# Kernel tuning notes

Measured on AMD Instinct MI355X. Metric: run time of the kernel, lower is better.

The kernel has to match this reference:

```python
import jax, jax.numpy as jnp
import numpy as np

B, NV, FD = 16, 128, 8192
T_TEMP = 0.2      # self.T
MARGIN = 1.0      # nn.TripletMarginLoss default
EPS = 1e-6        # pairwise_distance eps


def _l2norm(x):
    # torch F.normalize(dim=1): x / max(||x||, 1e-12)
    nrm = jnp.maximum(jnp.linalg.norm(x, axis=-1, keepdims=True), 1e-12)
    return x / nrm


def _ssl_parts(qb, kb, nb, num_gt):
    # qb,kb,nb: [NV, FD] flattened reid embeddings for one image
    qv = _l2norm(qb)[:num_gt]          # [g, FD]
    kv = _l2norm(kb)[:num_gt]          # [g, FD]
    nv = _l2norm(nb)                   # [NV, FD] (negatives are NOT sliced)
    g = num_gt
    S = qv @ kv.T                      # [g, g] all pairwise dots (replaces torch.dot loops)
    # similarity-matrix loss
    sm = jnp.sum((S - jnp.eye(g, dtype=S.dtype)) ** 2) / (g * g)
    # pairwise distances with torch eps convention: ||a - b + eps||_2
    # = sqrt(||a||^2 + ||b||^2 - 2 a.b + 2*eps*(sum(a)-sum(b)) + D*eps^2); ||a||=||b||=1
    sq = qv.sum(axis=1)                # [g]
    sk = kv.sum(axis=1)                # [g]
    const = FD * EPS * EPS
    d_qk = jnp.sqrt(jnp.maximum(2.0 - 2.0 * S + 2.0 * EPS * (sq[:, None] - sk[None, :]) + const, 0.0))
    d_kq = jnp.sqrt(jnp.maximum(2.0 - 2.0 * S.T + 2.0 * EPS * (sk[:, None] - sq[None, :]) + const, 0.0))
    off = 1.0 - jnp.eye(g, dtype=S.dtype)
    # triplet: anc=q_i,pos=k_i,neg=k_j  and  anc=k_i,pos=q_i,neg=q_j, j != i
    tri1 = jnp.sum(jax.nn.relu(jnp.diag(d_qk)[:, None] - d_qk + MARGIN) * off)
    tri2 = jnp.sum(jax.nn.relu(jnp.diag(d_kq)[:, None] - d_kq + MARGIN) * off)
    tri_sum = tri1 + tri2
    # cycle consistency: |q_i.k_j - k_i.q_j| = |S[i,j] - S[j,i]|
    cyc = jnp.sum(jnp.abs(S - S.T) * off) / (g * (g - 1))
    # InfoNCE: l_pos = q_i.k_i, l_neg = q @ n.T
    l_pos = jnp.diag(S)[:, None]       # [g, 1]
    l_neg = qv @ nv.T                  # [g, NV]
    logits = jnp.concatenate([l_pos, l_neg], axis=1) / T_TEMP
    ce = jnp.mean(jax.nn.logsumexp(logits, axis=1) - logits[:, 0])  # CE with labels=0
    return sm, tri_sum, cyc, ce / g


def setup_inputs() -> dict:
    key = jax.random.key(0)
    kq, kk, kn = jax.random.split(key, 3)
    q = jax.random.normal(kq, (B, NV, FD), dtype=jnp.float32)
    k = jax.random.normal(kk, (B, NV, FD), dtype=jnp.float32)
    n = jax.random.normal(kn, (B, NV, FD), dtype=jnp.float32)
    return {"q": q, "k": k, "n": n, "num_gt": NV}


def reference(q, k, n, num_gt):
    sm, tri, cyc, ce = jax.vmap(lambda a, b, c: _ssl_parts(a, b, c, num_gt))(q, k, n)
    tri_cnt = 2 * num_gt * (num_gt - 1)
    # original bug: tri_loss accumulates across batches while tri_cnt resets,
    # so each batch contributes cumsum(tri)[b] / tri_cnt
    ssl = jnp.sum(sm) + jnp.sum(jnp.cumsum(tri)) / tri_cnt + jnp.sum(cyc) + jnp.sum(ce)
    return ssl
```

## Files before the change

kernel.cpp:

```cpp
#include <hip/hip_runtime.h>
#include <cstdint>
#include <cstddef>

#define B_N   16
#define G_N   128
#define FD_N  8192
#define KSPLIT 16
#define KC    512
#define BK2   32
#define NITER 16

typedef unsigned short u16;
typedef u16  u16x4 __attribute__((ext_vector_type(4)));
typedef u16  u16x8 __attribute__((ext_vector_type(8)));
typedef __bf16 bf16x8 __attribute__((ext_vector_type(8)));
typedef float f32x16 __attribute__((ext_vector_type(16)));

#define QSUM_P   0
#define QSSQ_P   32768
#define KSUM_P   65536
#define KSSQ_P   98304
#define NSSQ_P   131072
#define SM_ROW   163840
#define CE_ROW   165888
#define S_OFF    167936
#define PART_OFF_F 430080

__device__ __forceinline__ u16 f2bf(float f) {
    uint32_t u = __float_as_uint(f);
    u += 0x7FFFu + ((u >> 16) & 1u);
    return (u16)(u >> 16);
}

#define LDS_BARRIER() asm volatile("s_waitcnt lgkmcnt(0)\n\ts_barrier" ::: "memory")

__global__ __launch_bounds__(512, 4)
void k_gemm(const float* __restrict__ q, const float* __restrict__ kM,
            const float* __restrict__ nM, float* __restrict__ ws)
{
    __shared__ __align__(16) u16 sA[G_N * BK2];
    __shared__ __align__(16) u16 sB[G_N * BK2];

    const int tid = threadIdx.x;
    const int blk = blockIdx.x;
    const int b    = blk >> 5;
    const int rem  = blk & 31;
    const int half = rem >> 4;
    const int kch  = rem & 15;

    const int r0 = tid >> 3;
    const int c8 = tid & 7;

    const size_t mat_off = (size_t)b * (G_N * FD_N) + (size_t)kch * KC + (size_t)(c8 * 4);
    const float* Ap = q + mat_off;
    const float* Bp = (half ? nM : kM) + mat_off;

    float4 a0[2], b0[2], a1[2], b1[2];
    float aS[2] = {0,0}, aQ[2] = {0,0}, bS[2] = {0,0}, bQ[2] = {0,0};

    #pragma unroll
    for (int i = 0; i < 2; ++i) {
        size_t ro = (size_t)(r0 + 64*i) * FD_N;
        a0[i] = *(const float4*)(Ap + ro);
        b0[i] = *(const float4*)(Bp + ro);
    }
    #pragma unroll
    for (int i = 0; i < 2; ++i) {
        size_t ro = (size_t)(r0 + 64*i) * FD_N + BK2;
        a1[i] = *(const float4*)(Ap + ro);
        b1[i] = *(const float4*)(Bp + ro);
    }

    const int lane  = tid & 63;
    const int wv    = tid >> 6;
    const int wm    = wv >> 2;
    const int wn    = wv & 3;
    const int khalf = lane >> 5;
    const int lrow  = lane & 31;
    const int rA0 = wm*64 + lrow;
    const int rB0 = wn*32 + lrow;

    int wof[2];
    #pragma unroll
    for (int i = 0; i < 2; ++i) {
        int row = r0 + 64*i;
        wof[i] = row*BK2 + 8*((c8>>1) ^ ((row>>1)&3)) + 4*(c8&1);
    }

    f32x16 acc[2];
    #pragma unroll
    for (int mb = 0; mb < 2; ++mb)
      #pragma unroll
      for (int e = 0; e < 16; ++e) acc[mb][e] = 0.f;

#define STORE_STAGE(AR, BR)                                                   \
    {                                                                         \
        _Pragma("unroll")                                                     \
        for (int i = 0; i < 2; ++i) {                                         \
            float4 v = AR[i];                                                 \
            aS[i] += v.x + v.y + v.z + v.w;                                   \
            aQ[i] += v.x*v.x + v.y*v.y + v.z*v.z + v.w*v.w;                   \
            u16x4 h; h[0]=f2bf(v.x); h[1]=f2bf(v.y); h[2]=f2bf(v.z); h[3]=f2bf(v.w); \
            *(u16x4*)(sA + wof[i]) = h;                                       \
            v = BR[i];                                                        \
            bS[i] += v.x + v.y + v.z + v.w;                                   \
            bQ[i] += v.x*v.x + v.y*v.y + v.z*v.z + v.w*v.w;                   \
            u16x4 h2; h2[0]=f2bf(v.x); h2[1]=f2bf(v.y); h2[2]=f2bf(v.z); h2[3]=f2bf(v.w); \
            *(u16x4*)(sB + wof[i]) = h2;                                      \
        }                                                                     \
    }

#define REFILL(AR, BR, KOFF)                                                  \
    {                                                                         \
        _Pragma("unroll")                                                     \
        for (int i = 0; i < 2; ++i) {                                         \
            size_t ro = (size_t)(r0 + 64*i) * FD_N + (KOFF);                  \
            AR[i] = *(const float4*)(Ap + ro);                                \
            BR[i] = *(const float4*)(Bp + ro);                                \
        }                                                                     \
    }

#define MFMA_PHASE()                                                          \
    {                                                                         \
        _Pragma("unroll")                                                     \
        for (int s = 0; s < 2; ++s) {                                         \
            int chunk = s*2 + khalf;                                          \
            bf16x8 af0, af1, bfv;                                             \
            { int row = rA0;                                                  \
              u16x8 raw = *(const u16x8*)(sA + row*BK2 + 8*(chunk ^ ((row>>1)&3))); \
              af0 = __builtin_bit_cast(bf16x8, raw); }                        \
            { int row = rA0 + 32;                                             \
              u16x8 raw = *(const u16x8*)(sA + row*BK2 + 8*(chunk ^ ((row>>1)&3))); \
              af1 = __builtin_bit_cast(bf16x8, raw); }                        \
            { int row = rB0;                                                  \
              u16x8 raw = *(const u16x8*)(sB + row*BK2 + 8*(chunk ^ ((row>>1)&3))); \
              bfv = __builtin_bit_cast(bf16x8, raw); }                        \
            acc[0] = __builtin_amdgcn_mfma_f32_32x32x16_bf16(af0, bfv, acc[0], 0, 0, 0); \
            acc[1] = __builtin_amdgcn_mfma_f32_32x32x16_bf16(af1, bfv, acc[1], 0, 0, 0); \
        }                                                                     \
    }

    for (int kb = 0; kb < NITER; kb += 2) {
        LDS_BARRIER();
        STORE_STAGE(a0, b0);
        LDS_BARRIER();
        if (kb + 2 < NITER) REFILL(a0, b0, (size_t)(kb+2)*BK2);
        MFMA_PHASE();
        LDS_BARRIER();
        STORE_STAGE(a1, b1);
        LDS_BARRIER();
        if (kb + 3 < NITER) REFILL(a1, b1, (size_t)(kb+3)*BK2);
        MFMA_PHASE();
    }

    u16* part = (u16*)(ws + PART_OFF_F) + ((size_t)blk << 14);
    #pragma unroll
    for (int mb = 0; mb < 2; ++mb) {
        int col = wn*32 + lrow;
        int rbase = wm*64 + mb*32 + 4*khalf;
        #pragma unroll
        for (int reg = 0; reg < 16; ++reg) {
            int row = rbase + (reg & 3) + 8*(reg >> 2);
            part[row*G_N + col] = f2bf(acc[mb][reg]);
        }
    }

    #pragma unroll
    for (int i = 0; i < 2; ++i) {
        float sa = aS[i], qa = aQ[i], sb = bS[i], qb = bQ[i];
        #pragma unroll
        for (int m = 4; m >= 1; m >>= 1) {
            sa += __shfl_xor(sa, m, 64); qa += __shfl_xor(qa, m, 64);
            sb += __shfl_xor(sb, m, 64); qb += __shfl_xor(qb, m, 64);
        }
        if (c8 == 0) {
            int o = kch*2048 + b*G_N + (r0 + 64*i);
            if (half == 0) {
                ws[QSUM_P + o] = sa; ws[QSSQ_P + o] = qa;
                ws[KSUM_P + o] = sb; ws[KSSQ_P + o] = qb;
            } else {
                ws[NSSQ_P + o] = qb;
            }
        }
    }
}

__global__ __launch_bounds__(256)
void k_red2(float* __restrict__ ws, float* __restrict__ out)
{
    const int blk  = blockIdx.x;
    const int b    = blk >> 4;
    const int half = (blk >> 3) & 1;
    const int rg   = blk & 7;
    const int t    = threadIdx.x;
    const int lr   = t >> 4;
    const int i    = rg*16 + lr;
    const int c8   = t & 15;
    __shared__ float nrm[128];
    __shared__ float invq_s[16];

    if (blk == 0 && t == 0) out[0] = 0.f;

    if (t < 128) {
        float ss = 0.f;
        const float* p = ws + (half ? NSSQ_P : KSSQ_P) + b*G_N + t;
        #pragma unroll
        for (int kc2 = 0; kc2 < KSPLIT; ++kc2) ss += p[kc2*2048];
        nrm[t] = 1.f / fmaxf(sqrtf(ss), 1e-12f);
    } else if (t < 144) {
        float ss = 0.f;
        const float* p = ws + QSSQ_P + b*G_N + rg*16 + (t - 128);
        #pragma unroll
        for (int kc2 = 0; kc2 < KSPLIT; ++kc2) ss += p[kc2*2048];
        invq_s[t-128] = 1.f / fmaxf(sqrtf(ss), 1e-12f);
    }
    __syncthreads();

    const u16* part = (const u16*)(ws + PART_OFF_F);
    float s[8] = {0,0,0,0,0,0,0,0};
    #pragma unroll
    for (int kc2 = 0; kc2 < KSPLIT; ++kc2) {
        size_t idx = ((size_t)(b*32 + half*16 + kc2) << 14) + i*G_N + c8*8;
        u16x8 h = *(const u16x8*)(part + idx);
        #pragma unroll
        for (int e = 0; e < 8; ++e)
            s[e] += __uint_as_float(((uint32_t)h[e]) << 16);
    }
    const float iq = invq_s[lr];
    if (half == 0) {
        float smacc = 0.f;
        float S8[8];
        #pragma unroll
        for (int e = 0; e < 8; ++e) {
            int j = c8*8 + e;
            S8[e] = s[e] * iq * nrm[j];
            float d = S8[e] - (j == i ? 1.f : 0.f);
            smacc += d*d;
        }
        float* Sp = ws + S_OFF + (size_t)b*16384 + i*G_N + c8*8;
        float4 w0 = {S8[0],S8[1],S8[2],S8[3]};
        float4 w1 = {S8[4],S8[5],S8[6],S8[7]};
        *(float4*)Sp = w0; *(float4*)(Sp+4) = w1;
        #pragma unroll
        for (int m = 8; m >= 1; m >>= 1) smacc += __shfl_xor(smacc, m, 64);
        if (c8 == 0) ws[SM_ROW + b*G_N + i] = smacc;
    } else {
        float eacc = 0.f;
        #pragma unroll
        for (int e = 0; e < 8; ++e)
            eacc += __expf(5.f * s[e] * iq * nrm[c8*8+e]);
        #pragma unroll
        for (int m = 8; m >= 1; m >>= 1) eacc += __shfl_xor(eacc, m, 64);
        if (c8 == 0) ws[CE_ROW + b*G_N + i] = eacc;
    }
}

__global__ __launch_bounds__(256)
void k_epi(float* __restrict__ ws, float* __restrict__ out)
{
    const int blk = blockIdx.x;
    const int b   = blk >> 3;
    const int i0  = (blk & 7) * 16;
    const int t   = threadIdx.x;
    __shared__ float sqv[128], skv[128], ddq[128], ddk[128];
    __shared__ float rbuf[4];
    const float c0 = (float)FD_N * 1e-6f * 1e-6f;

    const float* S = ws + S_OFF + (size_t)b * 16384;
    if (t < 128) {
        float qs=0, qq=0, ks=0, kq=0;
        #pragma unroll
        for (int kc2 = 0; kc2 < KSPLIT; ++kc2) {
            int o = kc2*2048 + b*G_N + t;
            qs += ws[QSUM_P + o]; qq += ws[QSSQ_P + o];
            ks += ws[KSUM_P + o]; kq += ws[KSSQ_P + o];
        }
        float iq = 1.f/fmaxf(sqrtf(qq),1e-12f);
        float ik = 1.f/fmaxf(sqrtf(kq),1e-12f);
        float sq = qs*iq, sk = ks*ik;
        sqv[t]=sq; skv[t]=sk;
        float Stt = S[t*G_N + t];
        ddq[t] = sqrtf(fmaxf(2.f - 2.f*Stt + 2e-6f*(sq-sk) + c0, 0.f));
        ddk[t] = sqrtf(fmaxf(2.f - 2.f*Stt + 2e-6f*(sk-sq) + c0, 0.f));
    }
    __syncthreads();

    float tri=0.f, cyc=0.f, ce=0.f, sm=0.f;
    #pragma unroll
    for (int p = 0; p < 8; ++p) {
        int idx = p*256 + t;
        int i = i0 + (idx >> 7), j = idx & 127;
        if (i != j) {
            float S_ij = S[i*G_N + j];
            float dqk = sqrtf(fmaxf(2.f - 2.f*S_ij + 2e-6f*(sqv[i]-skv[j]) + c0, 0.f));
            tri += fmaxf(ddq[i] - dqk + 1.f, 0.f);
            float dkq = sqrtf(fmaxf(2.f - 2.f*S_ij + 2e-6f*(skv[j]-sqv[i]) + c0, 0.f));
            tri += fmaxf(ddk[j] - dkq + 1.f, 0.f);
            cyc += fabsf(S_ij - S[j*G_N + i]);
        }
    }
    if (t < 16) {
        int r = i0 + t;
        float lp = 5.f * S[r*G_N + r];
        ce = __logf(ws[CE_ROW + b*G_N + r] + __expf(lp)) - lp;
        sm = ws[SM_ROW + b*G_N + r];
    }
    float contrib = sm * (1.f/16384.f) + cyc * (1.f/16256.f) + ce * (1.f/16384.f)
                  + (float)(B_N - b) * tri * (1.f/32512.f);
    #pragma unroll
    for (int m = 32; m >= 1; m >>= 1) contrib += __shfl_xor(contrib, m, 64);
    if ((t & 63) == 0) rbuf[t >> 6] = contrib;
    __syncthreads();
    if (t == 0) atomicAdd(out, rbuf[0] + rbuf[1] + rbuf[2] + rbuf[3]);
}

extern "C" void kernel_launch(void* const* d_in, const int* in_sizes, int n_in,
                              void* d_out, int out_size, void* d_ws, size_t ws_size,
                              hipStream_t stream)
{
    const float* q  = (const float*)d_in[0];
    const float* kM = (const float*)d_in[1];
    const float* nM = (const float*)d_in[2];
    float* ws  = (float*)d_ws;
    float* out = (float*)d_out;

    k_gemm<<<B_N * 2 * KSPLIT, 512, 0, stream>>>(q, kM, nM, ws);
    k_red2<<<256, 256, 0, stream>>>(ws, out);
    k_epi<<<128, 256, 0, stream>>>(ws, out);
}
```

Before: 219.2 us.

## Stream fp32 tiles to LDS via global_load_lds with double buffering

Result: no change. 219.6 us (+0.2%).

```diff
diff --git a/kernel.cpp b/kernel.cpp
--- a/kernel.cpp
+++ b/kernel.cpp
@@ -11,7 +11,6 @@
 #define NITER 16
 
 typedef unsigned short u16;
-typedef u16  u16x4 __attribute__((ext_vector_type(4)));
 typedef u16  u16x8 __attribute__((ext_vector_type(8)));
 typedef __bf16 bf16x8 __attribute__((ext_vector_type(8)));
 typedef float f32x16 __attribute__((ext_vector_type(16)));
@@ -32,14 +31,22 @@
     return (u16)(u >> 16);
 }
 
-#define LDS_BARRIER() asm volatile("s_waitcnt lgkmcnt(0)\n\ts_barrier" ::: "memory")
+__device__ __forceinline__ void load_lds16(const float* g, float* l) {
+    __builtin_amdgcn_global_load_lds(
+        (__attribute__((address_space(1))) void*)(g),
+        (__attribute__((address_space(3))) void*)(l),
+        16, 0, 0);
+}
+
+#define WAITV4() asm volatile("s_waitcnt vmcnt(4)" ::: "memory")
+#define WAITV0() asm volatile("s_waitcnt vmcnt(0)" ::: "memory")
 
 __global__ __launch_bounds__(512, 4)
 void k_gemm(const float* __restrict__ q, const float* __restrict__ kM,
             const float* __restrict__ nM, float* __restrict__ ws)
 {
-    __shared__ __align__(16) u16 sA[G_N * BK2];
-    __shared__ __align__(16) u16 sB[G_N * BK2];
+    __shared__ __align__(16) float sA[2][G_N * BK2];
+    __shared__ __align__(16) float sB[2][G_N * BK2];
 
     const int tid = threadIdx.x;
     const int blk = blockIdx.x;
@@ -47,29 +54,6 @@
     const int rem  = blk & 31;
     const int half = rem >> 4;
     const int kch  = rem & 15;
-
-    const int r0 = tid >> 3;
-    const int c8 = tid & 7;
-
-    const size_t mat_off = (size_t)b * (G_N * FD_N) + (size_t)kch * KC + (size_t)(c8 * 4);
-    const float* Ap = q + mat_off;
-    const float* Bp = (half ? nM : kM) + mat_off;
-
-    float4 a0[2], b0[2], a1[2], b1[2];
-    float aS[2] = {0,0}, aQ[2] = {0,0}, bS[2] = {0,0}, bQ[2] = {0,0};
-
-    #pragma unroll
-    for (int i = 0; i < 2; ++i) {
-        size_t ro = (size_t)(r0 + 64*i) * FD_N;
-        a0[i] = *(const float4*)(Ap + ro);
-        b0[i] = *(const float4*)(Bp + ro);
-    }
-    #pragma unroll
-    for (int i = 0; i < 2; ++i) {
-        size_t ro = (size_t)(r0 + 64*i) * FD_N + BK2;
-        a1[i] = *(const float4*)(Ap + ro);
-        b1[i] = *(const float4*)(Bp + ro);
-    }
 
     const int lane  = tid & 63;
     const int wv    = tid >> 6;
@@ -79,13 +63,61 @@
     const int lrow  = lane & 31;
     const int rA0 = wm*64 + lrow;
     const int rB0 = wn*32 + lrow;
-
-    int wof[2];
-    #pragma unroll
-    for (int i = 0; i < 2; ++i) {
-        int row = r0 + 64*i;
-        wof[i] = row*BK2 + 8*((c8>>1) ^ ((row>>1)&3)) + 4*(c8&1);
-    }
+    const bool statA = (wn == 0);
+    const bool statB = (wm == 0);
+
+    const size_t mat_off = (size_t)b * (G_N * FD_N) + (size_t)kch * KC;
+    const float* Ap = q + mat_off;
+    const float* Bp = (half ? nM : kM) + mat_off;
+
+    const int r0s = wv*16 + (lane >> 3);
+    const int r1s = r0s + 8;
+    const size_t goff0 = (size_t)r0s * FD_N + (size_t)(((lane & 7) ^ (r0s & 7)) << 2);
+    const size_t goff1 = (size_t)r1s * FD_N + (size_t)(((lane & 7) ^ (r1s & 7)) << 2);
+    const int lds0 = wv * 512;
+    const int lds1 = wv * 512 + 256;
+
+#define STAGE(ST, T) do {                                                     \
+        const size_t tof_ = (size_t)((T) * BK2);                              \
+        load_lds16(Ap + goff0 + tof_, &sA[ST][lds0]);                         \
+        load_lds16(Bp + goff0 + tof_, &sB[ST][lds0]);                         \
+        load_lds16(Ap + goff1 + tof_, &sA[ST][lds1]);                         \
+        load_lds16(Bp + goff1 + tof_, &sB[ST][lds1]);                         \
+    } while (0)
+
+#define LOADCVT(SP, R, CH, FR, EN, SS, QQ) do {                               \
+        const int x_ = (R) & 7;                                               \
+        const float* rp_ = (SP) + (R) * BK2;                                  \
+        float4 lo_ = *(const float4*)(rp_ + ((((CH)*2    ) ^ x_) << 2));      \
+        float4 hi_ = *(const float4*)(rp_ + ((((CH)*2 + 1) ^ x_) << 2));      \
+        if (EN) {                                                             \
+            SS += (lo_.x + lo_.y) + (lo_.z + lo_.w)                           \
+                + (hi_.x + hi_.y) + (hi_.z + hi_.w);                          \
+            QQ += lo_.x*lo_.x + lo_.y*lo_.y + lo_.z*lo_.z + lo_.w*lo_.w       \
+                + hi_.x*hi_.x + hi_.y*hi_.y + hi_.z*hi_.z + hi_.w*hi_.w;      \
+        }                                                                     \
+        u16x8 h_;                                                             \
+        h_[0]=f2bf(lo_.x); h_[1]=f2bf(lo_.y); h_[2]=f2bf(lo_.z); h_[3]=f2bf(lo_.w); \
+        h_[4]=f2bf(hi_.x); h_[5]=f2bf(hi_.y); h_[6]=f2bf(hi_.z); h_[7]=f2bf(hi_.w); \
+        FR = __builtin_bit_cast(bf16x8, h_);                                  \
+    } while (0)
+
+#define COMPUTE_PHASE(ST) do {                                                \
+        const float* sAp_ = &sA[ST][0];                                       \
+        const float* sBp_ = &sB[ST][0];                                       \
+        _Pragma("unroll")                                                     \
+        for (int s = 0; s < 2; ++s) {                                         \
+            const int ch = s*2 + khalf;                                       \
+            bf16x8 af0, af1, bfv;                                             \
+            LOADCVT(sAp_, rA0,      ch, af0, statA, aS0, aQ0);                \
+            LOADCVT(sAp_, rA0 + 32, ch, af1, statA, aS1, aQ1);                \
+            LOADCVT(sBp_, rB0,      ch, bfv, statB, bS0, bQ0);                \
+            acc[0] = __builtin_amdgcn_mfma_f32_32x32x16_bf16(af0, bfv, acc[0], 0, 0, 0); \
+            acc[1] = __builtin_amdgcn_mfma_f32_32x32x16_bf16(af1, bfv, acc[1], 0, 0, 0); \
+        }                                                                     \
+    } while (0)
+
+    float aS0 = 0.f, aQ0 = 0.f, aS1 = 0.f, aQ1 = 0.f, bS0 = 0.f, bQ0 = 0.f;
 
     f32x16 acc[2];
     #pragma unroll
@@ -93,65 +125,29 @@
       #pragma unroll
       for (int e = 0; e < 16; ++e) acc[mb][e] = 0.f;
 
-#define STORE_STAGE(AR, BR)                                                   \
-    {                                                                         \
-        _Pragma("unroll")                                                     \
-        for (int i = 0; i < 2; ++i) {                                         \
-            float4 v = AR[i];                                                 \
-            aS[i] += v.x + v.y + v.z + v.w;                                   \
-            aQ[i] += v.x*v.x + v.y*v.y + v.z*v.z + v.w*v.w;                   \
-            u16x4 h; h[0]=f2bf(v.x); h[1]=f2bf(v.y); h[2]=f2bf(v.z); h[3]=f2bf(v.w); \
-            *(u16x4*)(sA + wof[i]) = h;                                       \
-            v = BR[i];                                                        \
-            bS[i] += v.x + v.y + v.z + v.w;                                   \
-            bQ[i] += v.x*v.x + v.y*v.y + v.z*v.z + v.w*v.w;                   \
-            u16x4 h2; h2[0]=f2bf(v.x); h2[1]=f2bf(v.y); h2[2]=f2bf(v.z); h2[3]=f2bf(v.w); \
-            *(u16x4*)(sB + wof[i]) = h2;                                      \
-        }                                                                     \
-    }
-
-#define REFILL(AR, BR, KOFF)                                                  \
-    {                                                                         \
-        _Pragma("unroll")                                                     \
-        for (int i = 0; i < 2; ++i) {                                         \
-            size_t ro = (size_t)(r0 + 64*i) * FD_N + (KOFF);                  \
-            AR[i] = *(const float4*)(Ap + ro);                                \
-            BR[i] = *(const float4*)(Bp + ro);                                \
-        }                                                                     \
-    }
-
-#define MFMA_PHASE()                                                          \
-    {                                                                         \
-        _Pragma("unroll")                                                     \
-        for (int s = 0; s < 2; ++s) {                                         \
-            int chunk = s*2 + khalf;                                          \
-            bf16x8 af0, af1, bfv;                                             \
-            { int row = rA0;                                                  \
-              u16x8 raw = *(const u16x8*)(sA + row*BK2 + 8*(chunk ^ ((row>>1)&3))); \
-              af0 = __builtin_bit_cast(bf16x8, raw); }                        \
-            { int row = rA0 + 32;                                             \
-              u16x8 raw = *(const u16x8*)(sA + row*BK2 + 8*(chunk ^ ((row>>1)&3))); \
-              af1 = __builtin_bit_cast(bf16x8, raw); }                        \
-            { int row = rB0;                                                  \
-              u16x8 raw = *(const u16x8*)(sB + row*BK2 + 8*(chunk ^ ((row>>1)&3))); \
-              bfv = __builtin_bit_cast(bf16x8, raw); }                        \
-            acc[0] = __builtin_amdgcn_mfma_f32_32x32x16_bf16(af0, bfv, acc[0], 0, 0, 0); \
-            acc[1] = __builtin_amdgcn_mfma_f32_32x32x16_bf16(af1, bfv, acc[1], 0, 0, 0); \
-        }                                                                     \
-    }
-
-    for (int kb = 0; kb < NITER; kb += 2) {
-        LDS_BARRIER();
-        STORE_STAGE(a0, b0);
-        LDS_BARRIER();
-        if (kb + 2 < NITER) REFILL(a0, b0, (size_t)(kb+2)*BK2);
-        MFMA_PHASE();
-        LDS_BARRIER();
-        STORE_STAGE(a1, b1);
-        LDS_BARRIER();
-        if (kb + 3 < NITER) REFILL(a1, b1, (size_t)(kb+3)*BK2);
-        MFMA_PHASE();
-    }
+    STAGE(0, 0);
+    STAGE(1, 1);
+
+    for (int t = 0; t < 14; t += 2) {
+        WAITV4();
+        __builtin_amdgcn_s_barrier();
+        COMPUTE_PHASE(0);
+        __builtin_amdgcn_s_barrier();
+        STAGE(0, t + 2);
+
+        WAITV4();
+        __builtin_amdgcn_s_barrier();
+        COMPUTE_PHASE(1);
+        __builtin_amdgcn_s_barrier();
+        STAGE(1, t + 3);
+    }
+    WAITV4();
+    __builtin_amdgcn_s_barrier();
+    COMPUTE_PHASE(0);
+    __builtin_amdgcn_s_barrier();
+    WAITV0();
+    __builtin_amdgcn_s_barrier();
+    COMPUTE_PHASE(1);
 
     u16* part = (u16*)(ws + PART_OFF_F) + ((size_t)blk << 14);
     #pragma unroll
@@ -165,24 +161,26 @@
         }
     }
 
-    #pragma unroll
-    for (int i = 0; i < 2; ++i) {
-        float sa = aS[i], qa = aQ[i], sb = bS[i], qb = bQ[i];
-        #pragma unroll
-        for (int m = 4; m >= 1; m >>= 1) {
-            sa += __shfl_xor(sa, m, 64); qa += __shfl_xor(qa, m, 64);
-            sb += __shfl_xor(sb, m, 64); qb += __shfl_xor(qb, m, 64);
-        }
-        if (c8 == 0) {
-            int o = kch*2048 + b*G_N + (r0 + 64*i);
-            if (half == 0) {
-                ws[QSUM_P + o] = sa; ws[QSSQ_P + o] = qa;
-                ws[KSUM_P + o] = sb; ws[KSSQ_P + o] = qb;
-            } else {
-                ws[NSSQ_P + o] = qb;
-            }
-        }
-    }
+    if (statA) {
+        aS0 += __shfl_xor(aS0, 32, 64); aQ0 += __shfl_xor(aQ0, 32, 64);
+        aS1 += __shfl_xor(aS1, 32, 64); aQ1 += __shfl_xor(aQ1, 32, 64);
+        if (half == 0 && khalf == 0) {
+            int o = kch*2048 + b*G_N + wm*64 + lrow;
+            ws[QSUM_P + o]      = aS0; ws[QSSQ_P + o]      = aQ0;
+            ws[QSUM_P + o + 32] = aS1; ws[QSSQ_P + o + 32] = aQ1;
+        }
+    }
+    if (statB) {
+        bS0 += __shfl_xor(bS0, 32, 64); bQ0 += __shfl_xor(bQ0, 32, 64);
+        if (khalf == 0) {
+            int o = kch*2048 + b*G_N + wn*32 + lrow;
+            if (half == 0) { ws[KSUM_P + o] = bS0; ws[KSSQ_P + o] = bQ0; }
+            else           { ws[NSSQ_P + o] = bQ0; }
+        }
+    }
+#undef STAGE
+#undef LOADCVT
+#undef COMPUTE_PHASE
 }
 
 __global__ __launch_bounds__(256)
```

## Fuse q·kᵀ and q·nᵀ into one block tile to read q once

Applied to the files above, without the earlier changes.

Result: no change. 220.0 us (+0.4%).

```diff
diff --git a/kernel.cpp b/kernel.cpp
--- a/kernel.cpp
+++ b/kernel.cpp
@@ -7,11 +7,10 @@
 #define FD_N  8192
 #define KSPLIT 16
 #define KC    512
-#define BK2   32
-#define NITER 16
+#define BK    64
+#define NSTAGE 8
 
 typedef unsigned short u16;
-typedef u16  u16x4 __attribute__((ext_vector_type(4)));
 typedef u16  u16x8 __attribute__((ext_vector_type(8)));
 typedef __bf16 bf16x8 __attribute__((ext_vector_type(8)));
 typedef float f32x16 __attribute__((ext_vector_type(16)));
@@ -32,44 +31,19 @@
     return (u16)(u >> 16);
 }
 
-#define LDS_BARRIER() asm volatile("s_waitcnt lgkmcnt(0)\n\ts_barrier" ::: "memory")
-
-__global__ __launch_bounds__(512, 4)
+#define LGKM0_BAR() do { asm volatile("s_waitcnt lgkmcnt(0)" ::: "memory"); \
+                         __builtin_amdgcn_s_barrier(); } while (0)
+
+__global__ __launch_bounds__(512, 2)
 void k_gemm(const float* __restrict__ q, const float* __restrict__ kM,
             const float* __restrict__ nM, float* __restrict__ ws)
 {
-    __shared__ __align__(16) u16 sA[G_N * BK2];
-    __shared__ __align__(16) u16 sB[G_N * BK2];
+    __shared__ __align__(16) u16 smem[2 * 24576];
 
     const int tid = threadIdx.x;
     const int blk = blockIdx.x;
-    const int b    = blk >> 5;
-    const int rem  = blk & 31;
-    const int half = rem >> 4;
-    const int kch  = rem & 15;
-
-    const int r0 = tid >> 3;
-    const int c8 = tid & 7;
-
-    const size_t mat_off = (size_t)b * (G_N * FD_N) + (size_t)kch * KC + (size_t)(c8 * 4);
-    const float* Ap = q + mat_off;
-    const float* Bp = (half ? nM : kM) + mat_off;
-
-    float4 a0[2], b0[2], a1[2], b1[2];
-    float aS[2] = {0,0}, aQ[2] = {0,0}, bS[2] = {0,0}, bQ[2] = {0,0};
-
-    #pragma unroll
-    for (int i = 0; i < 2; ++i) {
-        size_t ro = (size_t)(r0 + 64*i) * FD_N;
-        a0[i] = *(const float4*)(Ap + ro);
-        b0[i] = *(const float4*)(Bp + ro);
-    }
-    #pragma unroll
-    for (int i = 0; i < 2; ++i) {
-        size_t ro = (size_t)(r0 + 64*i) * FD_N + BK2;
-        a1[i] = *(const float4*)(Ap + ro);
-        b1[i] = *(const float4*)(Bp + ro);
-    }
+    const int b   = blk >> 4;
+    const int kch = blk & 15;
 
     const int lane  = tid & 63;
     const int wv    = tid >> 6;
@@ -77,112 +51,147 @@
     const int wn    = wv & 3;
     const int khalf = lane >> 5;
     const int lrow  = lane & 31;
-    const int rA0 = wm*64 + lrow;
-    const int rB0 = wn*32 + lrow;
-
-    int wof[2];
-    #pragma unroll
-    for (int i = 0; i < 2; ++i) {
-        int row = r0 + 64*i;
-        wof[i] = row*BK2 + 8*((c8>>1) ^ ((row>>1)&3)) + 4*(c8&1);
-    }
-
-    f32x16 acc[2];
-    #pragma unroll
-    for (int mb = 0; mb < 2; ++mb)
+    const int g     = lane >> 4;
+    const int cc    = lane & 15;
+
+    const size_t mat_off = (size_t)b * (G_N * FD_N) + (size_t)kch * KC;
+    const float* Ap = q + mat_off;
+    const float* Bw = (wv < 4 ? kM : nM) + mat_off;
+
+    float4 La[4], Lb[8];
+    float sA_[4] = {0,0,0,0}, qA_[4] = {0,0,0,0};
+    float sB_[8] = {0,0,0,0,0,0,0,0}, qB_[8] = {0,0,0,0,0,0,0,0};
+
+    f32x16 acc[2][2];
+    #pragma unroll
+    for (int m = 0; m < 2; ++m)
       #pragma unroll
-      for (int e = 0; e < 16; ++e) acc[mb][e] = 0.f;
-
-#define STORE_STAGE(AR, BR)                                                   \
-    {                                                                         \
-        _Pragma("unroll")                                                     \
-        for (int i = 0; i < 2; ++i) {                                         \
-            float4 v = AR[i];                                                 \
-            aS[i] += v.x + v.y + v.z + v.w;                                   \
-            aQ[i] += v.x*v.x + v.y*v.y + v.z*v.z + v.w*v.w;                   \
-            u16x4 h; h[0]=f2bf(v.x); h[1]=f2bf(v.y); h[2]=f2bf(v.z); h[3]=f2bf(v.w); \
-            *(u16x4*)(sA + wof[i]) = h;                                       \
-            v = BR[i];                                                        \
-            bS[i] += v.x + v.y + v.z + v.w;                                   \
-            bQ[i] += v.x*v.x + v.y*v.y + v.z*v.z + v.w*v.w;                   \
-            u16x4 h2; h2[0]=f2bf(v.x); h2[1]=f2bf(v.y); h2[2]=f2bf(v.z); h2[3]=f2bf(v.w); \
-            *(u16x4*)(sB + wof[i]) = h2;                                      \
-        }                                                                     \
-    }
-
-#define REFILL(AR, BR, KOFF)                                                  \
-    {                                                                         \
-        _Pragma("unroll")                                                     \
-        for (int i = 0; i < 2; ++i) {                                         \
-            size_t ro = (size_t)(r0 + 64*i) * FD_N + (KOFF);                  \
-            AR[i] = *(const float4*)(Ap + ro);                                \
-            BR[i] = *(const float4*)(Bp + ro);                                \
-        }                                                                     \
-    }
-
-#define MFMA_PHASE()                                                          \
-    {                                                                         \
-        _Pragma("unroll")                                                     \
-        for (int s = 0; s < 2; ++s) {                                         \
-            int chunk = s*2 + khalf;                                          \
-            bf16x8 af0, af1, bfv;                                             \
-            { int row = rA0;                                                  \
-              u16x8 raw = *(const u16x8*)(sA + row*BK2 + 8*(chunk ^ ((row>>1)&3))); \
-              af0 = __builtin_bit_cast(bf16x8, raw); }                        \
-            { int row = rA0 + 32;                                             \
-              u16x8 raw = *(const u16x8*)(sA + row*BK2 + 8*(chunk ^ ((row>>1)&3))); \
-              af1 = __builtin_bit_cast(bf16x8, raw); }                        \
-            { int row = rB0;                                                  \
-              u16x8 raw = *(const u16x8*)(sB + row*BK2 + 8*(chunk ^ ((row>>1)&3))); \
-              bfv = __builtin_bit_cast(bf16x8, raw); }                        \
-            acc[0] = __builtin_amdgcn_mfma_f32_32x32x16_bf16(af0, bfv, acc[0], 0, 0, 0); \
-            acc[1] = __builtin_amdgcn_mfma_f32_32x32x16_bf16(af1, bfv, acc[1], 0, 0, 0); \
-        }                                                                     \
-    }
-
-    for (int kb = 0; kb < NITER; kb += 2) {
-        LDS_BARRIER();
-        STORE_STAGE(a0, b0);
-        LDS_BARRIER();
-        if (kb + 2 < NITER) REFILL(a0, b0, (size_t)(kb+2)*BK2);
-        MFMA_PHASE();
-        LDS_BARRIER();
-        STORE_STAGE(a1, b1);
-        LDS_BARRIER();
-        if (kb + 3 < NITER) REFILL(a1, b1, (size_t)(kb+3)*BK2);
-        MFMA_PHASE();
-    }
-
-    u16* part = (u16*)(ws + PART_OFF_F) + ((size_t)blk << 14);
-    #pragma unroll
-    for (int mb = 0; mb < 2; ++mb) {
-        int col = wn*32 + lrow;
-        int rbase = wm*64 + mb*32 + 4*khalf;
+      for (int n = 0; n < 2; ++n)
+        #pragma unroll
+        for (int e = 0; e < 16; ++e) acc[m][n][e] = 0.f;
+
+#define ISSUE(S) do {                                                          \
+        const size_t ko_ = (size_t)((S)*BK + cc*4);                            \
+        _Pragma("unroll")                                                      \
+        for (int i = 0; i < 4; ++i)                                            \
+            La[i] = *(const float4*)(Ap + (size_t)(wv*16 + i*4 + g)*FD_N + ko_); \
+        _Pragma("unroll")                                                      \
+        for (int i = 0; i < 8; ++i)                                            \
+            Lb[i] = *(const float4*)(Bw + (size_t)(wn*32 + i*4 + g)*FD_N + ko_); \
+    } while (0)
+
+#define CVTWRITE(BUF) do {                                                     \
+        u16* dA_ = smem + (BUF)*24576;                                         \
+        u16* dB_ = dA_ + 8192;                                                 \
+        _Pragma("unroll")                                                      \
+        for (int i = 0; i < 4; ++i) {                                          \
+            const int r_ = wv*16 + i*4 + g;                                    \
+            float4 v = La[i];                                                  \
+            sA_[i] += (v.x + v.y) + (v.z + v.w);                               \
+            qA_[i] += v.x*v.x + v.y*v.y + v.z*v.z + v.w*v.w;                   \
+            uint2 p;                                                           \
+            p.x = (uint32_t)f2bf(v.x) | ((uint32_t)f2bf(v.y) << 16);           \
+            p.y = (uint32_t)f2bf(v.z) | ((uint32_t)f2bf(v.w) << 16);           \
+            *(uint2*)(dA_ + r_*64 + ((cc ^ ((r_&7)<<1)) << 2)) = p;            \
+        }                                                                      \
+        _Pragma("unroll")                                                      \
+        for (int i = 0; i < 8; ++i) {                                          \
+            const int r_  = wn*32 + i*4 + g;                                   \
+            const int rl_ = r_ + (wv < 4 ? 0 : 128);                           \
+            float4 v = Lb[i];                                                  \
+            sB_[i] += (v.x + v.y) + (v.z + v.w);                               \
+            qB_[i] += v.x*v.x + v.y*v.y + v.z*v.z + v.w*v.w;                   \
+            uint2 p;                                                           \
+            p.x = (uint32_t)f2bf(v.x) | ((uint32_t)f2bf(v.y) << 16);           \
+            p.y = (uint32_t)f2bf(v.z) | ((uint32_t)f2bf(v.w) << 16);           \
+            *(uint2*)(dB_ + rl_*64 + ((cc ^ ((rl_&7)<<1)) << 2)) = p;          \
+        }                                                                      \
+    } while (0)
+
+#define FRAG(DP, R, KCH)                                                       \
+    __builtin_bit_cast(bf16x8, *(const u16x8*)((DP) + (R)*64 +                 \
+        ((((KCH)*2 + khalf) ^ ((R)&7)) << 3)))
+
+#define COMPUTE(BUF) do {                                                      \
+        const u16* dA_ = smem + (BUF)*24576;                                   \
+        const u16* dB_ = dA_ + 8192;                                           \
+        __builtin_amdgcn_s_setprio(1);                                         \
+        _Pragma("unroll")                                                      \
+        for (int kc = 0; kc < 4; ++kc) {                                       \
+            bf16x8 a0_ = FRAG(dA_, wm*64 +      lrow, kc);                     \
+            bf16x8 a1_ = FRAG(dA_, wm*64 + 32 + lrow, kc);                     \
+            bf16x8 b0_ = FRAG(dB_, wn*64 +      lrow, kc);                     \
+            bf16x8 b1_ = FRAG(dB_, wn*64 + 32 + lrow, kc);                     \
+            acc[0][0] = __builtin_amdgcn_mfma_f32_32x32x16_bf16(a0_, b0_, acc[0][0], 0,0,0); \
+            acc[0][1] = __builtin_amdgcn_mfma_f32_32x32x16_bf16(a0_, b1_, acc[0][1], 0,0,0); \
+            acc[1][0] = __builtin_amdgcn_mfma_f32_32x32x16_bf16(a1_, b0_, acc[1][0], 0,0,0); \
+            acc[1][1] = __builtin_amdgcn_mfma_f32_32x32x16_bf16(a1_, b1_, acc[1][1], 0,0,0); \
+        }                                                                      \
+        __builtin_amdgcn_s_setprio(0);                                         \
+    } while (0)
+
+    ISSUE(0);
+    CVTWRITE(0);
+    LGKM0_BAR();
+
+    for (int s = 0; s < NSTAGE; ++s) {
+        if (s + 1 < NSTAGE) ISSUE(s + 1);
+        COMPUTE(s & 1);
+        if (s + 1 < NSTAGE) {
+            LGKM0_BAR();
+            CVTWRITE((s + 1) & 1);
+            LGKM0_BAR();
+        }
+    }
+
+    u16* part = (u16*)(ws + PART_OFF_F);
+    #pragma unroll
+    for (int m = 0; m < 2; ++m)
+      #pragma unroll
+      for (int n = 0; n < 2; ++n) {
+        const int colg = wn*64 + n*32 + lrow;
+        const int ho   = colg >> 7;
+        const int col  = colg & 127;
+        u16* pb = part + (size_t)(b*2 + ho) * 262144;
+        const int rbase = wm*64 + m*32 + 4*khalf;
         #pragma unroll
         for (int reg = 0; reg < 16; ++reg) {
-            int row = rbase + (reg & 3) + 8*(reg >> 2);
-            part[row*G_N + col] = f2bf(acc[mb][reg]);
-        }
-    }
-
-    #pragma unroll
-    for (int i = 0; i < 2; ++i) {
-        float sa = aS[i], qa = aQ[i], sb = bS[i], qb = bQ[i];
-        #pragma unroll
-        for (int m = 4; m >= 1; m >>= 1) {
-            sa += __shfl_xor(sa, m, 64); qa += __shfl_xor(qa, m, 64);
-            sb += __shfl_xor(sb, m, 64); qb += __shfl_xor(qb, m, 64);
-        }
-        if (c8 == 0) {
-            int o = kch*2048 + b*G_N + (r0 + 64*i);
-            if (half == 0) {
-                ws[QSUM_P + o] = sa; ws[QSSQ_P + o] = qa;
-                ws[KSUM_P + o] = sb; ws[KSSQ_P + o] = qb;
-            } else {
-                ws[NSSQ_P + o] = qb;
-            }
-        }
-    }
+            const int row = rbase + (reg & 3) + 8*(reg >> 2);
+            pb[(row*16 + kch)*128 + col] = f2bf(acc[m][n][reg]);
+        }
+      }
+
+    #pragma unroll
+    for (int i = 0; i < 4; ++i)
+        #pragma unroll
+        for (int msk = 8; msk >= 1; msk >>= 1) {
+            sA_[i] += __shfl_xor(sA_[i], msk, 64);
+            qA_[i] += __shfl_xor(qA_[i], msk, 64);
+        }
+    #pragma unroll
+    for (int i = 0; i < 8; ++i)
+        #pragma unroll
+        for (int msk = 8; msk >= 1; msk >>= 1) {
+            sB_[i] += __shfl_xor(sB_[i], msk, 64);
+            qB_[i] += __shfl_xor(qB_[i], msk, 64);
+        }
+    if (cc == 0) {
+        #pragma unroll
+        for (int i = 0; i < 4; ++i) {
+            const int o = kch*2048 + b*G_N + (wv*16 + i*4 + g);
+            ws[QSUM_P + o] = sA_[i]; ws[QSSQ_P + o] = qA_[i];
+        }
+        #pragma unroll
+        for (int i = 0; i < 8; ++i) {
+            const int o = kch*2048 + b*G_N + (wn*32 + i*4 + g);
+            if (wv < 4) { ws[KSUM_P + o] = sB_[i]; ws[KSSQ_P + o] = qB_[i]; }
+            else        { ws[NSSQ_P + o] = qB_[i]; }
+        }
+    }
+#undef ISSUE
+#undef CVTWRITE
+#undef FRAG
+#undef COMPUTE
 }
 
 __global__ __launch_bounds__(256)
@@ -216,12 +225,11 @@
     }
     __syncthreads();
 
-    const u16* part = (const u16*)(ws + PART_OFF_F);
+    const u16* part = (const u16*)(ws + PART_OFF_F) + (size_t)(b*2 + half) * 262144;
     float s[8] = {0,0,0,0,0,0,0,0};
     #pragma unroll
     for (int kc2 = 0; kc2 < KSPLIT; ++kc2) {
-        size_t idx = ((size_t)(b*32 + half*16 + kc2) << 14) + i*G_N + c8*8;
-        u16x8 h = *(const u16x8*)(part + idx);
+        u16x8 h = *(const u16x8*)(part + (size_t)(i*16 + kc2)*128 + c8*8);
         #pragma unroll
         for (int e = 0; e < 8; ++e)
             s[e] += __uint_as_float(((uint32_t)h[e]) << 16);
@@ -324,7 +332,7 @@
     float* ws  = (float*)d_ws;
     float* out = (float*)d_out;
 
-    k_gemm<<<B_N * 2 * KSPLIT, 512, 0, stream>>>(q, kM, nM, ws);
+    k_gemm<<<B_N * KSPLIT, 512, 0, stream>>>(q, kM, nM, ws);
     k_red2<<<256, 256, 0, stream>>>(ws, out);
     k_epi<<<128, 256, 0, stream>>>(ws, out);
 }
```
